# Performance work log

Hardware: AMD Instinct MI355X
Metric: run time of the kernel (lower is better)

Reference implementation:

```python
import jax, jax.numpy as jnp
import numpy as np

N, F_T, F_P = 10000, 128, 64
MAIN_CH, SEC_CH = 7, 32


def _glorot(key, shape):
    fan_in, fan_out = shape[0], shape[1]
    lim = np.sqrt(6.0 / (fan_in + fan_out))
    return jax.random.uniform(key, shape, jnp.float32, -lim, lim)


def setup_inputs() -> dict:
    key = jax.random.key(0)
    ks = jax.random.split(key, 16)
    return {
        "temporal_features": jax.random.normal(ks[0], (N, F_T), jnp.float32),
        "A": jax.random.uniform(ks[1], (N, N), jnp.float32) / 100.0,
        "path_features": jax.random.normal(ks[2], (N, F_P), jnp.float32),
        # secondary ARMAConv: in F_T -> SEC_CH
        "Ws1": _glorot(ks[3], (F_T, SEC_CH)),
        "Ws2": _glorot(ks[4], (F_T, SEC_CH)),
        "bs": jnp.zeros((SEC_CH,), jnp.float32),
        # main2 ARMAConv: in SEC_CH+F_P -> MAIN_CH
        "Wm2a": _glorot(ks[5], (SEC_CH + F_P, MAIN_CH)),
        "Wm2b": _glorot(ks[6], (SEC_CH + F_P, MAIN_CH)),
        "bm2": jnp.zeros((MAIN_CH,), jnp.float32),
        # main ARMAConv: in F_T+F_P -> MAIN_CH
        "Wma": _glorot(ks[7], (F_T + F_P, MAIN_CH)),
        "Wmb": _glorot(ks[8], (F_T + F_P, MAIN_CH)),
        "bm": jnp.zeros((MAIN_CH,), jnp.float32),
        # scalar combine weights (v_bias_out init 1.0, v_bias_out2 init 0.0;
        # use small random values so both branches carry gradient)
        "v1": jax.random.normal(ks[9], (), jnp.float32) + 1.0,
        "v2": jax.random.normal(ks[10], (), jnp.float32),
    }


def _arma_gcs(x, A, W1, W2, b):
    # one ARMA graph-conv step (iterations=1, order=1, dropout off at eval):
    # A @ (x W1) + x W2 + b
    return A @ (x @ W1) + x @ W2 + b


def reference(temporal_features, A, path_features,
              Ws1, Ws2, bs, Wm2a, Wm2b, bm2, Wma, Wmb, bm, v1, v2):
    # secondary conv: gcn_activation=relu, activation=relu -> relu once
    sec = jax.nn.relu(_arma_gcs(temporal_features, A, Ws1, Ws2, bs))
    sec = jnp.concatenate([sec, path_features], axis=-1)          # [N, SEC+F_P]
    main_sec = _arma_gcs(sec, A, Wm2a, Wm2b, bm2)                 # [N, MAIN_CH]
    main_in = jnp.concatenate([temporal_features, path_features], axis=-1)
    main = _arma_gcs(main_in, A, Wma, Wmb, bm)                    # [N, MAIN_CH]
    # stack([v2*main, v1*main_sec], -1).mean(-1) then softmax
    combined = 0.5 * (v2 * main + v1 * main_sec)
    return jax.nn.softmax(combined, axis=-1)
```

## Files before the change

kernel.cpp:

```cpp
#include <hip/hip_runtime.h>
#include <stdint.h>
#include <math.h>

#define N_NODES 10000
#define NPAD 10048
#define KZ 8
#define NTILES 157

using short8 = __attribute__((ext_vector_type(8))) short;
using f32x4  = __attribute__((ext_vector_type(4))) float;

__device__ __forceinline__ uint32_t fbits(float x){ union{float f;uint32_t u;} v; v.f=x; return v.u; }
__device__ __forceinline__ float    fval(uint32_t u){ union{float f;uint32_t u;} v; v.u=u; return v.f; }

__device__ __forceinline__ void split1(float a, uint16_t& h, uint16_t& l){
  uint32_t ua = fbits(a);
  float lo = a - fval(ua & 0xFFFF0000u);
  h = (uint16_t)(ua >> 16);
  l = (uint16_t)(fbits(lo) >> 16);
}

__device__ __forceinline__ void split2pack(float x, float y, uint32_t& hp, uint32_t& lp){
  uint32_t ux = fbits(x), uy = fbits(y);
  float lx = x - fval(ux & 0xFFFF0000u);
  float ly = y - fval(uy & 0xFFFF0000u);
  hp = (uy & 0xFFFF0000u) | (ux >> 16);
  lp = (fbits(ly) & 0xFFFF0000u) | (fbits(lx) >> 16);
}

__global__ __launch_bounds__(256) void k1(
    const float* __restrict__ T, const float* __restrict__ P,
    const float* __restrict__ Ws1, const float* __restrict__ Ws2,
    const float* __restrict__ bs, const float* __restrict__ Wma,
    const float* __restrict__ Wmb, const float* __restrict__ bm,
    uint16_t* __restrict__ Yth, uint16_t* __restrict__ Ytl,
    float* __restrict__ Z2, float* __restrict__ Zm) {
  __shared__ float Xl[16 * 192];
  __shared__ float RedY[16 * 7], RedZ[16 * 7];
  int t = threadIdx.x;
  int r0 = blockIdx.x * 16;
  for (int s = t; s < 768; s += 256) {
    int r = s / 48, c4 = (s % 48) * 4;
    const float* src = (c4 < 128) ? &T[(size_t)(r0 + r) * 128 + c4]
                                  : &P[(size_t)(r0 + r) * 64 + (c4 - 128)];
    *(float4*)&Xl[r * 192 + c4] = *(const float4*)src;
  }
  __syncthreads();
  {
    int c = t & 31, r = t >> 5;
    float y0 = 0, z0 = 0, y1 = 0, z1 = 0;
    const float* x0 = &Xl[r * 192];
    const float* x1 = &Xl[(r + 8) * 192];
    #pragma unroll 8
    for (int k = 0; k < 128; ++k) {
      float w1 = Ws1[k * 32 + c], w2 = Ws2[k * 32 + c];
      float a0 = x0[k], a1 = x1[k];
      y0 += a0 * w1; z0 += a0 * w2;
      y1 += a1 * w1; z1 += a1 * w2;
    }
    int rowA = r0 + r, rowB = r0 + r + 8;
    float bsv = bs[c];
    Z2[rowA * 32 + c] = z0 + bsv;
    Z2[rowB * 32 + c] = z1 + bsv;
    uint16_t h, l;
    split1(y0, h, l); Yth[c * NPAD + rowA] = h; Ytl[c * NPAD + rowA] = l;
    split1(y1, h, l); Yth[c * NPAD + rowB] = h; Ytl[c * NPAD + rowB] = l;
  }
  int u = t & 15, r = t >> 4;
  int j = u % 7, half = u / 7;
  float ym = 0, zm = 0;
  if (u < 14) {
    int kb = half * 96;
    const float* xr = &Xl[r * 192];
    #pragma unroll 4
    for (int i = 0; i < 96; ++i) {
      int k = kb + i;
      float wa = Wma[k * 7 + j], wb = Wmb[k * 7 + j];
      float xv = xr[k];
      ym += xv * wa; zm += xv * wb;
    }
    if (half == 1) { RedY[r * 7 + j] = ym; RedZ[r * 7 + j] = zm; }
  }
  __syncthreads();
  if (u < 7) {
    ym += RedY[r * 7 + j]; zm += RedZ[r * 7 + j];
    int row = r0 + r;
    uint16_t h, l;
    split1(ym, h, l);
    Yth[(32 + j) * NPAD + row] = h; Ytl[(32 + j) * NPAD + row] = l;
    Zm[row * 7 + j] = zm + bm[j];
  }
}

template<int NCF, int NC, int CST>
__global__ __launch_bounds__(256) void k_spmm(
    const float* __restrict__ A, const uint16_t* __restrict__ Yth,
    const uint16_t* __restrict__ Ytl, float* __restrict__ Sacc) {
  __shared__ uint16_t Ah[64 * 72];
  __shared__ uint16_t Al[64 * 72];
  __shared__ uint16_t Yh[NCF * 16 * 72];
  __shared__ uint16_t Yl[NCF * 16 * 72];
  int t = threadIdx.x;
  int r0 = blockIdx.x * 64;
  int kz = blockIdx.y;
  int w = t >> 6, lane = t & 63;
  int m = lane & 15, q = lane >> 4;
  f32x4 acc[NCF];
  #pragma unroll
  for (int f = 0; f < NCF; ++f) acc[f] = (f32x4){0.f, 0.f, 0.f, 0.f};

  for (int tile = kz; tile < NTILES; tile += KZ) {
    int kt = tile * 64;
    __syncthreads();
    #pragma unroll
    for (int jj = 0; jj < 4; ++jj) {
      int fi = t + 256 * jj;
      int rr = fi >> 4, c4 = (fi & 15) * 4;
      int row = r0 + rr, k = kt + c4;
      float4 v = make_float4(0.f, 0.f, 0.f, 0.f);
      if (row < N_NODES && k < N_NODES)
        v = *(const float4*)&A[(size_t)row * N_NODES + k];
      uint32_t h0, l0, h1, l1;
      split2pack(v.x, v.y, h0, l0);
      split2pack(v.z, v.w, h1, l1);
      uint2 hh; hh.x = h0; hh.y = h1;
      uint2 ll; ll.x = l0; ll.y = l1;
      *(uint2*)&Ah[rr * 72 + c4] = hh;
      *(uint2*)&Al[rr * 72 + c4] = ll;
    }
    for (int s = t; s < NCF * 16 * 32; s += 256) {
      int c = s >> 5, kk = s & 31;
      int k2i = kt + 2 * kk;
      uint32_t vh = 0, vl = 0;
      if (c < NC && k2i < N_NODES) {
        vh = *(const uint32_t*)&Yth[(size_t)c * NPAD + k2i];
        vl = *(const uint32_t*)&Ytl[(size_t)c * NPAD + k2i];
      }
      *(uint32_t*)&Yh[c * 72 + 2 * kk] = vh;
      *(uint32_t*)&Yl[c * 72 + 2 * kk] = vl;
    }
    __syncthreads();
    #pragma unroll
    for (int ks = 0; ks < 2; ++ks) {
      int ko = ks * 32 + q * 8;
      short8 ah = *(const short8*)&Ah[(16 * w + m) * 72 + ko];
      short8 al = *(const short8*)&Al[(16 * w + m) * 72 + ko];
      #pragma unroll
      for (int f = 0; f < NCF; ++f) {
        short8 yh = *(const short8*)&Yh[(16 * f + m) * 72 + ko];
        short8 yl = *(const short8*)&Yl[(16 * f + m) * 72 + ko];
        acc[f] = __builtin_amdgcn_mfma_f32_16x16x32_bf16(ah, yh, acc[f], 0, 0, 0);
        acc[f] = __builtin_amdgcn_mfma_f32_16x16x32_bf16(ah, yl, acc[f], 0, 0, 0);
        acc[f] = __builtin_amdgcn_mfma_f32_16x16x32_bf16(al, yh, acc[f], 0, 0, 0);
      }
    }
  }
  int rb = r0 + 16 * w + q * 4;
  #pragma unroll
  for (int f = 0; f < NCF; ++f) {
    int col = 16 * f + m;
    if (col < CST) {
      #pragma unroll
      for (int r4 = 0; r4 < 4; ++r4) {
        int row = rb + r4;
        if (row < N_NODES) atomicAdd(&Sacc[(size_t)row * CST + col], acc[f][r4]);
      }
    }
  }
}

__global__ __launch_bounds__(256) void k2b(
    const float* __restrict__ Sacc, const float* __restrict__ Z2,
    const float* __restrict__ Zm, const float* __restrict__ v2p,
    float* __restrict__ sec, float* __restrict__ M0) {
  int g = blockIdx.x * 256 + threadIdx.x;
  if (g >= N_NODES * 40) return;
  int row = g / 40, c = g % 40;
  if (c < 32) {
    float s = Sacc[g] + Z2[row * 32 + c];
    sec[row * 32 + c] = fmaxf(s, 0.f);
  } else if (c < 39) {
    int j = c - 32;
    float s = Sacc[g] + Zm[row * 7 + j];
    M0[row * 7 + j] = 0.5f * v2p[0] * s;
  }
}

__global__ __launch_bounds__(256) void k2c(
    const float* __restrict__ sec, const float* __restrict__ P,
    const float* __restrict__ Wm2a, const float* __restrict__ Wm2b,
    const float* __restrict__ bm2, const float* __restrict__ v1p,
    const float* __restrict__ M0,
    uint16_t* __restrict__ Y2th, uint16_t* __restrict__ Y2tl,
    float* __restrict__ C0) {
  __shared__ float Xc[16 * 96];
  __shared__ float RedY[16 * 7], RedZ[16 * 7];
  int t = threadIdx.x;
  int r0 = blockIdx.x * 16;
  for (int s = t; s < 384; s += 256) {
    int r = s / 24, c4 = (s % 24) * 4;
    const float* src = (c4 < 32) ? &sec[(size_t)(r0 + r) * 32 + c4]
                                 : &P[(size_t)(r0 + r) * 64 + (c4 - 32)];
    *(float4*)&Xc[r * 96 + c4] = *(const float4*)src;
  }
  __syncthreads();
  int u = t & 15, r = t >> 4;
  int j = u % 7, half = u / 7;
  float y = 0, z = 0;
  if (u < 14) {
    int kb = half * 48;
    const float* xr = &Xc[r * 96];
    #pragma unroll 4
    for (int i = 0; i < 48; ++i) {
      int k = kb + i;
      y += xr[k] * Wm2a[k * 7 + j];
      z += xr[k] * Wm2b[k * 7 + j];
    }
    if (half == 1) { RedY[r * 7 + j] = y; RedZ[r * 7 + j] = z; }
  }
  __syncthreads();
  if (u < 7) {
    y += RedY[r * 7 + j]; z += RedZ[r * 7 + j];
    int row = r0 + r;
    uint16_t h, l;
    split1(y, h, l);
    Y2th[j * NPAD + row] = h; Y2tl[j * NPAD + row] = l;
    C0[row * 7 + j] = M0[row * 7 + j] + 0.5f * v1p[0] * (z + bm2[j]);
  }
}

__global__ __launch_bounds__(256) void k3b(
    const float* __restrict__ S2, const float* __restrict__ C0,
    const float* __restrict__ v1p, float* __restrict__ out) {
  int row = blockIdx.x * 256 + threadIdx.x;
  if (row >= N_NODES) return;
  float v1h = 0.5f * v1p[0];
  float comb[7];
  float mx = -1e30f;
  #pragma unroll
  for (int j = 0; j < 7; ++j) {
    float cv = C0[row * 7 + j] + v1h * S2[row * 8 + j];
    comb[j] = cv; mx = fmaxf(mx, cv);
  }
  float sum = 0.f;
  #pragma unroll
  for (int j = 0; j < 7; ++j) { comb[j] = expf(comb[j] - mx); sum += comb[j]; }
  float inv = 1.f / sum;
  #pragma unroll
  for (int j = 0; j < 7; ++j) out[row * 7 + j] = comb[j] * inv;
}

extern "C" void kernel_launch(void* const* d_in, const int* in_sizes, int n_in,
                              void* d_out, int out_size, void* d_ws, size_t ws_size,
                              hipStream_t stream) {
  const float* T    = (const float*)d_in[0];
  const float* A    = (const float*)d_in[1];
  const float* P    = (const float*)d_in[2];
  const float* Ws1  = (const float*)d_in[3];
  const float* Ws2  = (const float*)d_in[4];
  const float* bs   = (const float*)d_in[5];
  const float* Wm2a = (const float*)d_in[6];
  const float* Wm2b = (const float*)d_in[7];
  const float* bm2  = (const float*)d_in[8];
  const float* Wma  = (const float*)d_in[9];
  const float* Wmb  = (const float*)d_in[10];
  const float* bm   = (const float*)d_in[11];
  const float* v1   = (const float*)d_in[12];
  const float* v2   = (const float*)d_in[13];
  float* out = (float*)d_out;

  float* ws = (float*)d_ws;
  float* Sacc = ws;
  float* S2   = Sacc + 400000;
  float* Z2   = S2 + 80000;
  float* Zm   = Z2 + 320000;
  float* sec  = Zm + 70000;
  float* M0   = sec + 320000;
  float* C0   = M0 + 70000;
  uint16_t* Yth  = (uint16_t*)(C0 + 70000);
  uint16_t* Ytl  = Yth + 40 * NPAD;
  uint16_t* Y2th = Ytl + 40 * NPAD;
  uint16_t* Y2tl = Y2th + 8 * NPAD;

  hipMemsetAsync(Sacc, 0, (size_t)(400000 + 80000) * sizeof(float), stream);

  hipLaunchKernelGGL(k1, dim3(625), dim3(256), 0, stream,
                     T, P, Ws1, Ws2, bs, Wma, Wmb, bm, Yth, Ytl, Z2, Zm);
  hipLaunchKernelGGL((k_spmm<3, 39, 40>), dim3(NTILES, KZ), dim3(256), 0, stream,
                     A, Yth, Ytl, Sacc);
  hipLaunchKernelGGL(k2b, dim3((N_NODES * 40 + 255) / 256), dim3(256), 0, stream,
                     Sacc, Z2, Zm, v2, sec, M0);
  hipLaunchKernelGGL(k2c, dim3(625), dim3(256), 0, stream,
                     sec, P, Wm2a, Wm2b, bm2, v1, M0, Y2th, Y2tl, C0);
  hipLaunchKernelGGL((k_spmm<1, 7, 8>), dim3(NTILES, KZ), dim3(256), 0, stream,
                     A, Y2th, Y2tl, S2);
  hipLaunchKernelGGL(k3b, dim3((N_NODES + 255) / 256), dim3(256), 0, stream,
                     S2, C0, v1, out);
}
```

Baseline: 792.2 us.

## Load A directly into MFMA registers, contiguous K-splits, partial-sum buffers instead of atomics

The dense A·Y kernel now skips the LDS staging and the barriers. Each lane loads its A row and its Y column fragments straight from global memory into MFMA operand registers and splits them into bf16 hi/lo there. The K split becomes contiguous chunks of 10 tiles over 16 z-blocks, with a guarded tail tile. Per-split partial results go to separate buffers that the consumer kernels reduce, replacing the atomics and the memset. This trades LDS traffic and sync for uncoalesced per-lane global loads and a larger partial-sum buffer read in the reduction kernels.

After: 830.4 us. 1.05x slower.

```diff
diff --git a/kernel.cpp b/kernel.cpp
--- a/kernel.cpp
+++ b/kernel.cpp
@@ -2,10 +2,11 @@
 #include <stdint.h>
 #include <math.h>
 
-#define N_NODES 10000
+#define AN 10000
 #define NPAD 10048
-#define KZ 8
+#define KZ 16
 #define NTILES 157
+#define TPB 10
 
 using short8 = __attribute__((ext_vector_type(8))) short;
 using f32x4  = __attribute__((ext_vector_type(4))) float;
@@ -20,12 +21,15 @@
   l = (uint16_t)(fbits(lo) >> 16);
 }
 
-__device__ __forceinline__ void split2pack(float x, float y, uint32_t& hp, uint32_t& lp){
-  uint32_t ux = fbits(x), uy = fbits(y);
-  float lx = x - fval(ux & 0xFFFF0000u);
-  float ly = y - fval(uy & 0xFFFF0000u);
-  hp = (uy & 0xFFFF0000u) | (ux >> 16);
-  lp = (fbits(ly) & 0xFFFF0000u) | (fbits(lx) >> 16);
+__device__ __forceinline__ void split8(const float4& a, const float4& b, short8& h, short8& l){
+  float v[8] = {a.x, a.y, a.z, a.w, b.x, b.y, b.z, b.w};
+  #pragma unroll
+  for (int i = 0; i < 8; ++i) {
+    uint32_t u = fbits(v[i]);
+    h[i] = (short)(u >> 16);
+    float r = v[i] - fval(u & 0xFFFF0000u);
+    l[i] = (short)(fbits(r) >> 16);
+  }
 }
 
 __global__ __launch_bounds__(256) void k1(
@@ -75,9 +79,8 @@
     #pragma unroll 4
     for (int i = 0; i < 96; ++i) {
       int k = kb + i;
-      float wa = Wma[k * 7 + j], wb = Wmb[k * 7 + j];
-      float xv = xr[k];
-      ym += xv * wa; zm += xv * wb;
+      ym += xr[k] * Wma[k * 7 + j];
+      zm += xr[k] * Wmb[k * 7 + j];
     }
     if (half == 1) { RedY[r * 7 + j] = ym; RedZ[r * 7 + j] = zm; }
   }
@@ -95,94 +98,105 @@
 template<int NCF, int NC, int CST>
 __global__ __launch_bounds__(256) void k_spmm(
     const float* __restrict__ A, const uint16_t* __restrict__ Yth,
-    const uint16_t* __restrict__ Ytl, float* __restrict__ Sacc) {
-  __shared__ uint16_t Ah[64 * 72];
-  __shared__ uint16_t Al[64 * 72];
-  __shared__ uint16_t Yh[NCF * 16 * 72];
-  __shared__ uint16_t Yl[NCF * 16 * 72];
+    const uint16_t* __restrict__ Ytl, float* __restrict__ Spart) {
   int t = threadIdx.x;
+  int w = t >> 6, lane = t & 63;
+  int m = lane & 15, q = lane >> 4;
   int r0 = blockIdx.x * 64;
   int kz = blockIdx.y;
-  int w = t >> 6, lane = t & 63;
-  int m = lane & 15, q = lane >> 4;
+  int row = r0 + 16 * w + m;
+  int rowc = row < AN ? row : AN - 1;
+  const float* arow = A + (size_t)rowc * AN;
+  const uint16_t* yhp[NCF];
+  const uint16_t* ylp[NCF];
+  #pragma unroll
+  for (int f = 0; f < NCF; ++f) {
+    int col = 16 * f + m; if (col > NC - 1) col = NC - 1;
+    yhp[f] = Yth + (size_t)col * NPAD;
+    ylp[f] = Ytl + (size_t)col * NPAD;
+  }
   f32x4 acc[NCF];
   #pragma unroll
   for (int f = 0; f < NCF; ++f) acc[f] = (f32x4){0.f, 0.f, 0.f, 0.f};
 
-  for (int tile = kz; tile < NTILES; tile += KZ) {
+  int t0 = kz * TPB;
+  int t1 = t0 + TPB; if (t1 > NTILES) t1 = NTILES;
+  int te = t1 < NTILES - 1 ? t1 : NTILES - 1;
+  int kq = q * 8;
+
+  for (int tile = t0; tile < te; ++tile) {
     int kt = tile * 64;
-    __syncthreads();
-    #pragma unroll
-    for (int jj = 0; jj < 4; ++jj) {
-      int fi = t + 256 * jj;
-      int rr = fi >> 4, c4 = (fi & 15) * 4;
-      int row = r0 + rr, k = kt + c4;
-      float4 v = make_float4(0.f, 0.f, 0.f, 0.f);
-      if (row < N_NODES && k < N_NODES)
-        v = *(const float4*)&A[(size_t)row * N_NODES + k];
-      uint32_t h0, l0, h1, l1;
-      split2pack(v.x, v.y, h0, l0);
-      split2pack(v.z, v.w, h1, l1);
-      uint2 hh; hh.x = h0; hh.y = h1;
-      uint2 ll; ll.x = l0; ll.y = l1;
-      *(uint2*)&Ah[rr * 72 + c4] = hh;
-      *(uint2*)&Al[rr * 72 + c4] = ll;
-    }
-    for (int s = t; s < NCF * 16 * 32; s += 256) {
-      int c = s >> 5, kk = s & 31;
-      int k2i = kt + 2 * kk;
-      uint32_t vh = 0, vl = 0;
-      if (c < NC && k2i < N_NODES) {
-        vh = *(const uint32_t*)&Yth[(size_t)c * NPAD + k2i];
-        vl = *(const uint32_t*)&Ytl[(size_t)c * NPAD + k2i];
-      }
-      *(uint32_t*)&Yh[c * 72 + 2 * kk] = vh;
-      *(uint32_t*)&Yl[c * 72 + 2 * kk] = vl;
-    }
-    __syncthreads();
     #pragma unroll
     for (int ks = 0; ks < 2; ++ks) {
-      int ko = ks * 32 + q * 8;
-      short8 ah = *(const short8*)&Ah[(16 * w + m) * 72 + ko];
-      short8 al = *(const short8*)&Al[(16 * w + m) * 72 + ko];
+      int k = kt + ks * 32 + kq;
+      float4 a0 = *(const float4*)(arow + k);
+      float4 a1 = *(const float4*)(arow + k + 4);
+      short8 ah, al;
+      split8(a0, a1, ah, al);
       #pragma unroll
       for (int f = 0; f < NCF; ++f) {
-        short8 yh = *(const short8*)&Yh[(16 * f + m) * 72 + ko];
-        short8 yl = *(const short8*)&Yl[(16 * f + m) * 72 + ko];
-        acc[f] = __builtin_amdgcn_mfma_f32_16x16x32_bf16(ah, yh, acc[f], 0, 0, 0);
-        acc[f] = __builtin_amdgcn_mfma_f32_16x16x32_bf16(ah, yl, acc[f], 0, 0, 0);
-        acc[f] = __builtin_amdgcn_mfma_f32_16x16x32_bf16(al, yh, acc[f], 0, 0, 0);
+        short8 vyh = *(const short8*)(yhp[f] + k);
+        short8 vyl = *(const short8*)(ylp[f] + k);
+        acc[f] = __builtin_amdgcn_mfma_f32_16x16x32_bf16(ah, vyh, acc[f], 0, 0, 0);
+        acc[f] = __builtin_amdgcn_mfma_f32_16x16x32_bf16(ah, vyl, acc[f], 0, 0, 0);
+        acc[f] = __builtin_amdgcn_mfma_f32_16x16x32_bf16(al, vyh, acc[f], 0, 0, 0);
       }
     }
   }
+  if (t1 == NTILES) {
+    int kt = (NTILES - 1) * 64;
+    #pragma unroll
+    for (int ks = 0; ks < 2; ++ks) {
+      int k = kt + ks * 32 + kq;
+      float4 a0 = make_float4(0.f, 0.f, 0.f, 0.f);
+      float4 a1 = make_float4(0.f, 0.f, 0.f, 0.f);
+      if (k + 8 <= AN) {
+        a0 = *(const float4*)(arow + k);
+        a1 = *(const float4*)(arow + k + 4);
+      }
+      short8 ah, al;
+      split8(a0, a1, ah, al);
+      #pragma unroll
+      for (int f = 0; f < NCF; ++f) {
+        short8 vyh = *(const short8*)(yhp[f] + k);
+        short8 vyl = *(const short8*)(ylp[f] + k);
+        acc[f] = __builtin_amdgcn_mfma_f32_16x16x32_bf16(ah, vyh, acc[f], 0, 0, 0);
+        acc[f] = __builtin_amdgcn_mfma_f32_16x16x32_bf16(ah, vyl, acc[f], 0, 0, 0);
+        acc[f] = __builtin_amdgcn_mfma_f32_16x16x32_bf16(al, vyh, acc[f], 0, 0, 0);
+      }
+    }
+  }
+  float* outp = Spart + (size_t)kz * AN * CST;
   int rb = r0 + 16 * w + q * 4;
   #pragma unroll
   for (int f = 0; f < NCF; ++f) {
     int col = 16 * f + m;
-    if (col < CST) {
+    if (col < NC) {
       #pragma unroll
       for (int r4 = 0; r4 < 4; ++r4) {
-        int row = rb + r4;
-        if (row < N_NODES) atomicAdd(&Sacc[(size_t)row * CST + col], acc[f][r4]);
+        int rr = rb + r4;
+        if (rr < AN) outp[(size_t)rr * CST + col] = acc[f][r4];
       }
     }
   }
 }
 
 __global__ __launch_bounds__(256) void k2b(
-    const float* __restrict__ Sacc, const float* __restrict__ Z2,
+    const float* __restrict__ Spart, const float* __restrict__ Z2,
     const float* __restrict__ Zm, const float* __restrict__ v2p,
     float* __restrict__ sec, float* __restrict__ M0) {
   int g = blockIdx.x * 256 + threadIdx.x;
-  if (g >= N_NODES * 40) return;
-  int row = g / 40, c = g % 40;
+  if (g >= AN * 40) return;
+  int row = g / 40, c = g - row * 40;
+  if (c >= 39) return;
+  float s = 0.f;
+  #pragma unroll
+  for (int kz = 0; kz < KZ; ++kz) s += Spart[(size_t)kz * AN * 40 + g];
   if (c < 32) {
-    float s = Sacc[g] + Z2[row * 32 + c];
-    sec[row * 32 + c] = fmaxf(s, 0.f);
-  } else if (c < 39) {
+    sec[row * 32 + c] = fmaxf(s + Z2[row * 32 + c], 0.f);
+  } else {
     int j = c - 32;
-    float s = Sacc[g] + Zm[row * 7 + j];
-    M0[row * 7 + j] = 0.5f * v2p[0] * s;
+    M0[row * 7 + j] = 0.5f * v2p[0] * (s + Zm[row * 7 + j]);
   }
 }
 
@@ -230,16 +244,26 @@
 }
 
 __global__ __launch_bounds__(256) void k3b(
-    const float* __restrict__ S2, const float* __restrict__ C0,
+    const float* __restrict__ S2part, const float* __restrict__ C0,
     const float* __restrict__ v1p, float* __restrict__ out) {
   int row = blockIdx.x * 256 + threadIdx.x;
-  if (row >= N_NODES) return;
+  if (row >= AN) return;
+  float s[8];
+  #pragma unroll
+  for (int j = 0; j < 8; ++j) s[j] = 0.f;
+  for (int kz = 0; kz < KZ; ++kz) {
+    const float* p = &S2part[(size_t)kz * AN * 8 + (size_t)row * 8];
+    float4 u0 = *(const float4*)p;
+    float4 u1 = *(const float4*)(p + 4);
+    s[0] += u0.x; s[1] += u0.y; s[2] += u0.z; s[3] += u0.w;
+    s[4] += u1.x; s[5] += u1.y; s[6] += u1.z;
+  }
   float v1h = 0.5f * v1p[0];
   float comb[7];
   float mx = -1e30f;
   #pragma unroll
   for (int j = 0; j < 7; ++j) {
-    float cv = C0[row * 7 + j] + v1h * S2[row * 8 + j];
+    float cv = C0[row * 7 + j] + v1h * s[j];
     comb[j] = cv; mx = fmaxf(mx, cv);
   }
   float sum = 0.f;
@@ -270,30 +294,28 @@
   float* out = (float*)d_out;
 
   float* ws = (float*)d_ws;
-  float* Sacc = ws;
-  float* S2   = Sacc + 400000;
-  float* Z2   = S2 + 80000;
-  float* Zm   = Z2 + 320000;
-  float* sec  = Zm + 70000;
-  float* M0   = sec + 320000;
-  float* C0   = M0 + 70000;
-  uint16_t* Yth  = (uint16_t*)(C0 + 70000);
-  uint16_t* Ytl  = Yth + 40 * NPAD;
-  uint16_t* Y2th = Ytl + 40 * NPAD;
-  uint16_t* Y2tl = Y2th + 8 * NPAD;
-
-  hipMemsetAsync(Sacc, 0, (size_t)(400000 + 80000) * sizeof(float), stream);
+  float* Spart  = ws;
+  float* S2part = Spart + (size_t)KZ * AN * 40;
+  float* Z2     = S2part + (size_t)KZ * AN * 8;
+  float* Zm     = Z2 + (size_t)AN * 32;
+  float* sec    = Zm + (size_t)AN * 7;
+  float* M0     = sec + (size_t)AN * 32;
+  float* C0     = M0 + (size_t)AN * 7;
+  uint16_t* Yth  = (uint16_t*)(C0 + (size_t)AN * 7);
+  uint16_t* Ytl  = Yth + (size_t)40 * NPAD;
+  uint16_t* Y2th = Ytl + (size_t)40 * NPAD;
+  uint16_t* Y2tl = Y2th + (size_t)8 * NPAD;
 
   hipLaunchKernelGGL(k1, dim3(625), dim3(256), 0, stream,
                      T, P, Ws1, Ws2, bs, Wma, Wmb, bm, Yth, Ytl, Z2, Zm);
   hipLaunchKernelGGL((k_spmm<3, 39, 40>), dim3(NTILES, KZ), dim3(256), 0, stream,
-                     A, Yth, Ytl, Sacc);
-  hipLaunchKernelGGL(k2b, dim3((N_NODES * 40 + 255) / 256), dim3(256), 0, stream,
-                     Sacc, Z2, Zm, v2, sec, M0);
+                     A, Yth, Ytl, Spart);
+  hipLaunchKernelGGL(k2b, dim3((AN * 40 + 255) / 256), dim3(256), 0, stream,
+                     Spart, Z2, Zm, v2, sec, M0);
   hipLaunchKernelGGL(k2c, dim3(625), dim3(256), 0, stream,
                      sec, P, Wm2a, Wm2b, bm2, v1, M0, Y2th, Y2tl, C0);
   hipLaunchKernelGGL((k_spmm<1, 7, 8>), dim3(NTILES, KZ), dim3(256), 0, stream,
-                     A, Y2th, Y2tl, S2);
-  hipLaunchKernelGGL(k3b, dim3((N_NODES + 255) / 256), dim3(256), 0, stream,
-                     S2, C0, v1, out);
-}
+                     A, Y2th, Y2tl, S2part);
+  hipLaunchKernelGGL(k3b, dim3((AN + 255) / 256), dim3(256), 0, stream,
+                     S2part, C0, v1, out);
+}
```
